# Kernel optimization log

Hardware: AMD Instinct MI355X
Metric: run time of the kernel (lower is better)

The kernel has to match this reference:

```python
import jax, jax.numpy as jnp
import numpy as np

DIM = 768
HEADS = 12
HEAD_DIM = DIM // HEADS
SCALE = HEAD_DIM ** -0.5


def setup_inputs() -> dict:
    key = jax.random.key(0)
    ks = jax.random.split(key, 7)
    B, N, C = 4, 1024, DIM
    s = 0.02
    return {
        "x": jax.random.normal(ks[0], (B, N, C), dtype=jnp.float32),
        "attn_mask": jax.random.normal(ks[1], (B, N, N), dtype=jnp.float32) * 0.1,
        "w_qkv": jax.random.normal(ks[2], (3 * C, C), dtype=jnp.float32) * s,
        "w_proj": jax.random.normal(ks[3], (C, C), dtype=jnp.float32) * s,
        "b_proj": jnp.zeros((C,), dtype=jnp.float32),
        "w_pre": jax.random.normal(ks[4], (HEADS, HEADS), dtype=jnp.float32) * 0.2,
        "w_post": jax.random.normal(ks[5], (HEADS, HEADS), dtype=jnp.float32) * 0.2,
    }


def reference(x, attn_mask, w_qkv, w_proj, b_proj, w_pre, w_post):
    B, N, C = x.shape
    H, D = HEADS, HEAD_DIM
    qkv = (x @ w_qkv.T).reshape(B, N, 3, H, D)
    q, k, v = jnp.moveaxis(qkv, 2, 0)          # each [B, N, H, D]
    q = q.transpose(0, 2, 1, 3)                # [B, H, N, D]
    k = k.transpose(0, 2, 1, 3)
    v = v.transpose(0, 2, 1, 3)
    attn = jnp.einsum("bhnd,bhmd->bhnm", q, k) * SCALE
    attn = attn + attn_mask[:, None, :, :]
    # talking-heads pre-softmax mixing: Linear over head axis (y = x @ W.T)
    attn = jnp.einsum("bhnm,gh->bgnm", attn, w_pre)
    attn = jax.nn.softmax(attn, axis=-1)
    # talking-heads post-softmax mixing
    attn = jnp.einsum("bhnm,gh->bgnm", attn, w_post)
    out = jnp.einsum("bhnm,bhmd->bhnd", attn, v)   # [B, H, N, D]
    out = out.transpose(0, 2, 1, 3).reshape(B, N, C)
    return out @ w_proj.T + b_proj
```

## Files before the change

### kernel.cpp

```cpp
#include <hip/hip_runtime.h>
#include <hip/hip_bf16.h>

typedef __attribute__((ext_vector_type(8))) short bf16x8;
typedef __attribute__((ext_vector_type(8))) short s16x8;
typedef __attribute__((ext_vector_type(4))) float f32x4;
typedef unsigned short u16;

__device__ __forceinline__ u16 f2bf(float f){
  __hip_bfloat16 h = __float2bfloat16(f);
  return *reinterpret_cast<u16*>(&h);
}
__device__ __forceinline__ float bf2f(u16 u){
  __hip_bfloat16 h;
  *reinterpret_cast<u16*>(&h) = u;
  return __bfloat162float(h);
}

__global__ __launch_bounds__(256) void cvt3_kernel(
    const float* __restrict__ s0, u16* __restrict__ d0, int n0,
    const float* __restrict__ s1, u16* __restrict__ d1, int n1,
    const float* __restrict__ s2, u16* __restrict__ d2, int n2)
{
  int i = blockIdx.x*256 + threadIdx.x;
  const float* s; u16* d; int idx; float sc = 1.f;
  if (i < n0){ s = s0; d = d0; idx = i; }
  else if (i < n0 + n1){
    idx = i - n0; s = s1; d = d1;
    if (idx < 768*192) sc = 0.125f;
  } else if (i < n0 + n1 + n2){
    idx = i - n0 - n1; s = s2; d = d2;
  } else return;
  float4 v = reinterpret_cast<const float4*>(s)[idx];
  ushort4 o;
  o.x = f2bf(v.x*sc); o.y = f2bf(v.y*sc); o.z = f2bf(v.z*sc); o.w = f2bf(v.w*sc);
  reinterpret_cast<ushort4*>(d)[idx] = o;
}

template<int BM, int BN, int MODE>
__global__ __launch_bounds__(256) void gemm_bt(
    const u16* __restrict__ A, const u16* __restrict__ B,
    void* __restrict__ C0, void* __restrict__ C1, void* __restrict__ C2,
    const float* __restrict__ bias,
    int M, int N, int K, int lda, int ldb, long sA, long sB, long sC)
{
  constexpr int BK = 32, LDT = 40;
  __shared__ u16 As[BM*LDT];
  __shared__ u16 Bs[BN*LDT];
  const int z = blockIdx.z;
  const u16* Ab = A + (long)z * sA;
  const u16* Bb = B + (long)z * sB;
  const int bm = blockIdx.x * BM, bn = blockIdx.y * BN;
  const int tid = threadIdx.x, lane = tid & 63, wv = tid >> 6;
  constexpr int WM = BM/2, WN = BN/2, FM = WM/16, FN = WN/16;
  const int wm = (wv >> 1) * WM, wn = (wv & 1) * WN;
  const int quad = lane >> 4, cl = lane & 15;
  f32x4 acc[FM][FN];
  #pragma unroll
  for (int i=0;i<FM;i++)
    #pragma unroll
    for (int j=0;j<FN;j++){ f32x4 zr = {0.f,0.f,0.f,0.f}; acc[i][j] = zr; }
  constexpr int AIT = (BM*BK)/(8*256);
  constexpr int BIT = (BN*BK)/(8*256);

  for (int kb = 0; kb < K; kb += BK){
    __syncthreads();
    #pragma unroll
    for (int sL=0; sL<AIT; sL++){
      int e = tid + sL*256, r = e >> 2, c8 = (e & 3) * 8;
      *reinterpret_cast<float4*>(&As[r*LDT + c8]) =
        *reinterpret_cast<const float4*>(Ab + (long)(bm + r)*lda + kb + c8);
    }
    #pragma unroll
    for (int sL=0; sL<BIT; sL++){
      int e = tid + sL*256, r = e >> 2, c8 = (e & 3) * 8;
      *reinterpret_cast<float4*>(&Bs[r*LDT + c8]) =
        *reinterpret_cast<const float4*>(Bb + (long)(bn + r)*ldb + kb + c8);
    }
    __syncthreads();
    bf16x8 af[FM], bfr[FN];
    #pragma unroll
    for (int i=0;i<FM;i++)
      af[i] = *reinterpret_cast<const bf16x8*>(&As[(wm + i*16 + cl)*LDT + quad*8]);
    #pragma unroll
    for (int j=0;j<FN;j++)
      bfr[j] = *reinterpret_cast<const bf16x8*>(&Bs[(wn + j*16 + cl)*LDT + quad*8]);
    #pragma unroll
    for (int i=0;i<FM;i++)
      #pragma unroll
      for (int j=0;j<FN;j++)
        acc[i][j] = __builtin_amdgcn_mfma_f32_16x16x32_bf16(af[i], bfr[j], acc[i][j], 0, 0, 0);
  }

  #pragma unroll
  for (int i=0;i<FM;i++)
  #pragma unroll
  for (int j=0;j<FN;j++)
  #pragma unroll
  for (int r=0;r<4;r++){
    int gm = bm + wm + i*16 + quad*4 + r;
    int gn = bn + wn + j*16 + cl;
    float v = acc[i][j][r];
    if (MODE == 0){
      int b_ = gm >> 10, n_ = gm & 1023;
      int t3 = (gn >= 1536) ? 2 : ((gn >= 768) ? 1 : 0);
      int rem = gn - t3*768;
      int h = rem >> 6, d = rem & 63;
      u16 hv = f2bf(v);
      if (t3 == 0)      ((u16*)C0)[((long)((b_*12 + h)*1024 + n_))*64 + d] = hv;
      else if (t3 == 1) ((u16*)C1)[((long)((b_*12 + h)*1024 + n_))*64 + d] = hv;
      else              ((u16*)C2)[((long)((b_*12 + h)*64 + d))*1024 + n_] = hv;
    } else if (MODE == 1){
      ((u16*)C0)[(long)z*sC + (long)gm*N + gn] = f2bf(v);
    } else if (MODE == 2){
      int b_ = z / 12, h = z - b_*12;
      ((u16*)C0)[((long)((b_*1024 + gm)*12 + h))*64 + gn] = f2bf(v);
    } else {
      ((float*)C0)[(long)gm*N + gn] = v + bias[gn];
    }
  }
}

__global__ __launch_bounds__(64, 2) void mix_kernel(
    u16* __restrict__ S, const float* __restrict__ mask,
    const float* __restrict__ w_pre, const float* __restrict__ w_post)
{
  const int bid = blockIdx.x;
  const int b = bid >> 10, n = bid & 1023;
  const int l = threadIdx.x;
  const long base0 = (((long)(b*12))*1024 + n) * 1024;
  const int off0 = l*8, off1 = 512 + l*8;

  float smix[12][16];

  #pragma unroll
  for (int h=0; h<12; h++){
    const u16* sr = S + base0 + (long)h*1024*1024;
    bf16x8 v0 = *reinterpret_cast<const bf16x8*>(sr + off0);
    bf16x8 v1 = *reinterpret_cast<const bf16x8*>(sr + off1);
    float sv[16];
    #pragma unroll
    for (int j=0;j<8;j++){ sv[j] = bf2f((u16)v0[j]); sv[8+j] = bf2f((u16)v1[j]); }
    if (h == 0){
      #pragma unroll
      for (int g=0;g<12;g++){
        float w = w_pre[g*12];
        #pragma unroll
        for (int mi=0;mi<16;mi++) smix[g][mi] = w * sv[mi];
      }
    } else {
      #pragma unroll
      for (int g=0;g<12;g++){
        float w = w_pre[g*12 + h];
        #pragma unroll
        for (int mi=0;mi<16;mi++) smix[g][mi] += w * sv[mi];
      }
    }
  }

  {
    const float* mr = mask + ((long)(b*1024 + n))*1024;
    float mk[16];
    float4 a0 = *reinterpret_cast<const float4*>(mr + off0);
    float4 a1 = *reinterpret_cast<const float4*>(mr + off0 + 4);
    float4 b0 = *reinterpret_cast<const float4*>(mr + off1);
    float4 b1 = *reinterpret_cast<const float4*>(mr + off1 + 4);
    mk[0]=a0.x; mk[1]=a0.y; mk[2]=a0.z; mk[3]=a0.w;
    mk[4]=a1.x; mk[5]=a1.y; mk[6]=a1.z; mk[7]=a1.w;
    mk[8]=b0.x; mk[9]=b0.y; mk[10]=b0.z; mk[11]=b0.w;
    mk[12]=b1.x; mk[13]=b1.y; mk[14]=b1.z; mk[15]=b1.w;
    #pragma unroll
    for (int g=0;g<12;g++){
      float rs = 0.f;
      #pragma unroll
      for (int h=0;h<12;h++) rs += w_pre[g*12 + h];
      #pragma unroll
      for (int mi=0;mi<16;mi++) smix[g][mi] += rs * mk[mi];
    }
  }

  float M[12];
  #pragma unroll
  for (int g=0;g<12;g++){
    float a = fmaxf(smix[g][0], smix[g][1]);
    float c = fmaxf(smix[g][2], smix[g][3]);
    float e = fmaxf(smix[g][4], smix[g][5]);
    float f = fmaxf(smix[g][6], smix[g][7]);
    float a2 = fmaxf(smix[g][8], smix[g][9]);
    float c2 = fmaxf(smix[g][10], smix[g][11]);
    float e2 = fmaxf(smix[g][12], smix[g][13]);
    float f2 = fmaxf(smix[g][14], smix[g][15]);
    M[g] = fmaxf(fmaxf(fmaxf(a,c), fmaxf(e,f)), fmaxf(fmaxf(a2,c2), fmaxf(e2,f2)));
  }
  #pragma unroll
  for (int off=32; off>0; off>>=1)
    #pragma unroll
    for (int g=0;g<12;g++) M[g] = fmaxf(M[g], __shfl_xor(M[g], off));

  float L[12];
  #pragma unroll
  for (int g=0;g<12;g++){
    float sum = 0.f;
    #pragma unroll
    for (int mi=0;mi<16;mi++){
      float e = __expf(smix[g][mi] - M[g]);
      smix[g][mi] = e; sum += e;
    }
    L[g] = sum;
  }
  #pragma unroll
  for (int off=32; off>0; off>>=1)
    #pragma unroll
    for (int g=0;g<12;g++) L[g] += __shfl_xor(L[g], off);
  #pragma unroll
  for (int g=0;g<12;g++){
    float inv = 1.0f / L[g];
    #pragma unroll
    for (int mi=0;mi<16;mi++) smix[g][mi] *= inv;
  }

  #pragma unroll
  for (int h=0; h<12; h++){
    float o[16];
    {
      float w = w_post[h*12];
      #pragma unroll
      for (int mi=0;mi<16;mi++) o[mi] = w * smix[0][mi];
    }
    #pragma unroll
    for (int g=1;g<12;g++){
      float w = w_post[h*12 + g];
      #pragma unroll
      for (int mi=0;mi<16;mi++) o[mi] += w * smix[g][mi];
    }
    s16x8 st0, st1;
    #pragma unroll
    for (int j=0;j<8;j++){
      st0[j] = (short)f2bf(o[j]);
      st1[j] = (short)f2bf(o[8+j]);
    }
    u16* orow = S + base0 + (long)h*1024*1024;
    *reinterpret_cast<s16x8*>(orow + off0) = st0;
    *reinterpret_cast<s16x8*>(orow + off1) = st1;
  }
}

extern "C" void kernel_launch(void* const* d_in, const int* in_sizes, int n_in,
                              void* d_out, int out_size, void* d_ws, size_t ws_size,
                              hipStream_t stream)
{
  const float* x      = (const float*)d_in[0];
  const float* mask   = (const float*)d_in[1];
  const float* w_qkv  = (const float*)d_in[2];
  const float* w_proj = (const float*)d_in[3];
  const float* b_proj = (const float*)d_in[4];
  const float* w_pre  = (const float*)d_in[5];
  const float* w_post = (const float*)d_in[6];
  float* out = (float*)d_out;

  u16* xb     = (u16*)d_ws;
  u16* wqkvb  = xb     + 4096l*768;
  u16* wprojb = wqkvb  + 2304l*768;
  u16* Qb     = wprojb + 768l*768;
  u16* Kb     = Qb     + 48l*1024*64;
  u16* Vtb    = Kb     + 48l*1024*64;
  u16* tmpb   = Vtb    + 48l*1024*64;
  u16* Sb     = tmpb   + 4096l*768;
  size_t need = ((size_t)(Sb - xb) + 48ul*1024*1024) * sizeof(u16);
  if (ws_size < need) return;

  const int n0 = 4096*768/4, n1 = 2304*768/4, n2 = 768*768/4;
  cvt3_kernel<<<(n0+n1+n2 + 255)/256, 256, 0, stream>>>(x, xb, n0, w_qkv, wqkvb, n1,
                                                        w_proj, wprojb, n2);

  dim3 gq(4096/128, 2304/128, 1);
  gemm_bt<128,128,0><<<gq, 256, 0, stream>>>(xb, wqkvb, Qb, Kb, Vtb, nullptr,
      4096, 2304, 768, 768, 768, 0, 0, 0);

  dim3 gs(1024/128, 1024/128, 48);
  gemm_bt<128,128,1><<<gs, 256, 0, stream>>>(Qb, Kb, Sb, nullptr, nullptr, nullptr,
      1024, 1024, 64, 64, 64, 1024l*64, 1024l*64, 1024l*1024);

  mix_kernel<<<4096, 64, 0, stream>>>(Sb, mask, w_pre, w_post);

  dim3 gp(1024/128, 1, 48);
  gemm_bt<128,64,2><<<gp, 256, 0, stream>>>(Sb, Vtb, tmpb, nullptr, nullptr, nullptr,
      1024, 64, 1024, 1024, 1024, 1024l*1024, 64l*1024, 0);

  dim3 go(4096/128, 768/128, 1);
  gemm_bt<128,128,3><<<go, 256, 0, stream>>>(tmpb, wprojb, out, nullptr, nullptr, b_proj,
      4096, 768, 768, 768, 768, 0, 0, 0);
}
```

Measured before the change: 293.4 us.

## Use direct global-to-LDS loads, widen mix kernel to two waves, shrink PV tile

The GEMM tile loads now use the global_load_lds builtin to copy straight into shared memory, with the LDS padding removed (LDT 32), so tiles no longer pass through registers. The mix kernel now runs 128 threads per row with 8 elements each, combines the two waves' max and sum through shared memory, and converts bf16 with shifts. The PV GEMM switches to 64x64 tiles for more blocks. Together these aim to cut register pressure, raise occupancy and reduce load latency, at the cost of possible LDS bank conflicts from the unpadded layout.

```diff
diff --git a/kernel.cpp b/kernel.cpp
--- a/kernel.cpp
+++ b/kernel.cpp
@@ -5,15 +5,19 @@
 typedef __attribute__((ext_vector_type(8))) short s16x8;
 typedef __attribute__((ext_vector_type(4))) float f32x4;
 typedef unsigned short u16;
+typedef unsigned int u32;
 
 __device__ __forceinline__ u16 f2bf(float f){
   __hip_bfloat16 h = __float2bfloat16(f);
   return *reinterpret_cast<u16*>(&h);
 }
-__device__ __forceinline__ float bf2f(u16 u){
-  __hip_bfloat16 h;
-  *reinterpret_cast<u16*>(&h) = u;
-  return __bfloat162float(h);
+__device__ __forceinline__ float bflo(u32 w){ return __uint_as_float(w << 16); }
+__device__ __forceinline__ float bfhi(u32 w){ return __uint_as_float(w & 0xffff0000u); }
+
+__device__ __forceinline__ void gload_lds16(const u16* g, u16* l){
+  __builtin_amdgcn_global_load_lds(
+      (__attribute__((address_space(1))) u32*)g,
+      (__attribute__((address_space(3))) u32*)l, 16, 0, 0);
 }
 
 __global__ __launch_bounds__(256) void cvt3_kernel(
@@ -43,9 +47,9 @@
     const float* __restrict__ bias,
     int M, int N, int K, int lda, int ldb, long sA, long sB, long sC)
 {
-  constexpr int BK = 32, LDT = 40;
-  __shared__ u16 As[BM*LDT];
-  __shared__ u16 Bs[BN*LDT];
+  constexpr int BK = 32, LDT = 32;
+  __shared__ __align__(16) u16 As[BM*LDT];
+  __shared__ __align__(16) u16 Bs[BN*LDT];
   const int z = blockIdx.z;
   const u16* Ab = A + (long)z * sA;
   const u16* Bb = B + (long)z * sB;
@@ -67,14 +71,12 @@
     #pragma unroll
     for (int sL=0; sL<AIT; sL++){
       int e = tid + sL*256, r = e >> 2, c8 = (e & 3) * 8;
-      *reinterpret_cast<float4*>(&As[r*LDT + c8]) =
-        *reinterpret_cast<const float4*>(Ab + (long)(bm + r)*lda + kb + c8);
+      gload_lds16(Ab + (long)(bm + r)*lda + kb + c8, &As[e*8]);
     }
     #pragma unroll
     for (int sL=0; sL<BIT; sL++){
       int e = tid + sL*256, r = e >> 2, c8 = (e & 3) * 8;
-      *reinterpret_cast<float4*>(&Bs[r*LDT + c8]) =
-        *reinterpret_cast<const float4*>(Bb + (long)(bn + r)*ldb + kb + c8);
+      gload_lds16(Bb + (long)(bn + r)*ldb + kb + c8, &Bs[e*8]);
     }
     __syncthreads();
     bf16x8 af[FM], bfr[FN];
@@ -120,88 +122,87 @@
   }
 }
 
-__global__ __launch_bounds__(64, 2) void mix_kernel(
+__global__ __launch_bounds__(128) __attribute__((amdgpu_waves_per_eu(3,3)))
+void mix_kernel(
     u16* __restrict__ S, const float* __restrict__ mask,
     const float* __restrict__ w_pre, const float* __restrict__ w_post)
 {
   const int bid = blockIdx.x;
   const int b = bid >> 10, n = bid & 1023;
-  const int l = threadIdx.x;
+  const int t = threadIdx.x;
+  const int wv = t >> 6, lane = t & 63;
+  const int moff = t * 8;
   const long base0 = (((long)(b*12))*1024 + n) * 1024;
-  const int off0 = l*8, off1 = 512 + l*8;
-
-  float smix[12][16];
+
+  float smix[12][8];
 
   #pragma unroll
   for (int h=0; h<12; h++){
-    const u16* sr = S + base0 + (long)h*1024*1024;
-    bf16x8 v0 = *reinterpret_cast<const bf16x8*>(sr + off0);
-    bf16x8 v1 = *reinterpret_cast<const bf16x8*>(sr + off1);
-    float sv[16];
-    #pragma unroll
-    for (int j=0;j<8;j++){ sv[j] = bf2f((u16)v0[j]); sv[8+j] = bf2f((u16)v1[j]); }
+    uint4 raw = *reinterpret_cast<const uint4*>(S + base0 + (long)h*1024*1024 + moff);
+    float sv[8];
+    sv[0]=bflo(raw.x); sv[1]=bfhi(raw.x);
+    sv[2]=bflo(raw.y); sv[3]=bfhi(raw.y);
+    sv[4]=bflo(raw.z); sv[5]=bfhi(raw.z);
+    sv[6]=bflo(raw.w); sv[7]=bfhi(raw.w);
     if (h == 0){
       #pragma unroll
       for (int g=0;g<12;g++){
         float w = w_pre[g*12];
         #pragma unroll
-        for (int mi=0;mi<16;mi++) smix[g][mi] = w * sv[mi];
+        for (int mi=0;mi<8;mi++) smix[g][mi] = w * sv[mi];
       }
     } else {
       #pragma unroll
       for (int g=0;g<12;g++){
         float w = w_pre[g*12 + h];
         #pragma unroll
-        for (int mi=0;mi<16;mi++) smix[g][mi] += w * sv[mi];
+        for (int mi=0;mi<8;mi++) smix[g][mi] += w * sv[mi];
       }
     }
   }
 
   {
-    const float* mr = mask + ((long)(b*1024 + n))*1024;
-    float mk[16];
-    float4 a0 = *reinterpret_cast<const float4*>(mr + off0);
-    float4 a1 = *reinterpret_cast<const float4*>(mr + off0 + 4);
-    float4 b0 = *reinterpret_cast<const float4*>(mr + off1);
-    float4 b1 = *reinterpret_cast<const float4*>(mr + off1 + 4);
-    mk[0]=a0.x; mk[1]=a0.y; mk[2]=a0.z; mk[3]=a0.w;
-    mk[4]=a1.x; mk[5]=a1.y; mk[6]=a1.z; mk[7]=a1.w;
-    mk[8]=b0.x; mk[9]=b0.y; mk[10]=b0.z; mk[11]=b0.w;
-    mk[12]=b1.x; mk[13]=b1.y; mk[14]=b1.z; mk[15]=b1.w;
+    const float* mr = mask + ((long)(b*1024 + n))*1024 + moff;
+    float4 a0 = *reinterpret_cast<const float4*>(mr);
+    float4 a1 = *reinterpret_cast<const float4*>(mr + 4);
+    float mk[8] = {a0.x,a0.y,a0.z,a0.w,a1.x,a1.y,a1.z,a1.w};
     #pragma unroll
     for (int g=0;g<12;g++){
       float rs = 0.f;
       #pragma unroll
       for (int h=0;h<12;h++) rs += w_pre[g*12 + h];
       #pragma unroll
-      for (int mi=0;mi<16;mi++) smix[g][mi] += rs * mk[mi];
-    }
-  }
-
+      for (int mi=0;mi<8;mi++) smix[g][mi] += rs * mk[mi];
+    }
+  }
+
+  __shared__ float redM[2][12];
+  __shared__ float redS[2][12];
   float M[12];
   #pragma unroll
   for (int g=0;g<12;g++){
-    float a = fmaxf(smix[g][0], smix[g][1]);
-    float c = fmaxf(smix[g][2], smix[g][3]);
-    float e = fmaxf(smix[g][4], smix[g][5]);
-    float f = fmaxf(smix[g][6], smix[g][7]);
-    float a2 = fmaxf(smix[g][8], smix[g][9]);
-    float c2 = fmaxf(smix[g][10], smix[g][11]);
-    float e2 = fmaxf(smix[g][12], smix[g][13]);
-    float f2 = fmaxf(smix[g][14], smix[g][15]);
-    M[g] = fmaxf(fmaxf(fmaxf(a,c), fmaxf(e,f)), fmaxf(fmaxf(a2,c2), fmaxf(e2,f2)));
+    float a = fmaxf(fmaxf(smix[g][0], smix[g][1]), fmaxf(smix[g][2], smix[g][3]));
+    float c = fmaxf(fmaxf(smix[g][4], smix[g][5]), fmaxf(smix[g][6], smix[g][7]));
+    M[g] = fmaxf(a, c);
   }
   #pragma unroll
   for (int off=32; off>0; off>>=1)
     #pragma unroll
     for (int g=0;g<12;g++) M[g] = fmaxf(M[g], __shfl_xor(M[g], off));
+  if (lane == 0){
+    #pragma unroll
+    for (int g=0;g<12;g++) redM[wv][g] = M[g];
+  }
+  __syncthreads();
+  #pragma unroll
+  for (int g=0;g<12;g++) M[g] = fmaxf(redM[0][g], redM[1][g]);
 
   float L[12];
   #pragma unroll
   for (int g=0;g<12;g++){
     float sum = 0.f;
     #pragma unroll
-    for (int mi=0;mi<16;mi++){
+    for (int mi=0;mi<8;mi++){
       float e = __expf(smix[g][mi] - M[g]);
       smix[g][mi] = e; sum += e;
     }
@@ -211,36 +212,36 @@
   for (int off=32; off>0; off>>=1)
     #pragma unroll
     for (int g=0;g<12;g++) L[g] += __shfl_xor(L[g], off);
+  if (lane == 0){
+    #pragma unroll
+    for (int g=0;g<12;g++) redS[wv][g] = L[g];
+  }
+  __syncthreads();
   #pragma unroll
   for (int g=0;g<12;g++){
-    float inv = 1.0f / L[g];
-    #pragma unroll
-    for (int mi=0;mi<16;mi++) smix[g][mi] *= inv;
+    float inv = 1.0f / (redS[0][g] + redS[1][g]);
+    #pragma unroll
+    for (int mi=0;mi<8;mi++) smix[g][mi] *= inv;
   }
 
   #pragma unroll
   for (int h=0; h<12; h++){
-    float o[16];
+    float o[8];
     {
       float w = w_post[h*12];
       #pragma unroll
-      for (int mi=0;mi<16;mi++) o[mi] = w * smix[0][mi];
+      for (int mi=0;mi<8;mi++) o[mi] = w * smix[0][mi];
     }
     #pragma unroll
     for (int g=1;g<12;g++){
       float w = w_post[h*12 + g];
       #pragma unroll
-      for (int mi=0;mi<16;mi++) o[mi] += w * smix[g][mi];
-    }
-    s16x8 st0, st1;
-    #pragma unroll
-    for (int j=0;j<8;j++){
-      st0[j] = (short)f2bf(o[j]);
-      st1[j] = (short)f2bf(o[8+j]);
-    }
-    u16* orow = S + base0 + (long)h*1024*1024;
-    *reinterpret_cast<s16x8*>(orow + off0) = st0;
-    *reinterpret_cast<s16x8*>(orow + off1) = st1;
+      for (int mi=0;mi<8;mi++) o[mi] += w * smix[g][mi];
+    }
+    s16x8 st;
+    #pragma unroll
+    for (int j=0;j<8;j++) st[j] = (short)f2bf(o[j]);
+    *reinterpret_cast<s16x8*>(S + base0 + (long)h*1024*1024 + moff) = st;
   }
 }
 
@@ -280,10 +281,10 @@
   gemm_bt<128,128,1><<<gs, 256, 0, stream>>>(Qb, Kb, Sb, nullptr, nullptr, nullptr,
       1024, 1024, 64, 64, 64, 1024l*64, 1024l*64, 1024l*1024);
 
-  mix_kernel<<<4096, 64, 0, stream>>>(Sb, mask, w_pre, w_post);
-
-  dim3 gp(1024/128, 1, 48);
-  gemm_bt<128,64,2><<<gp, 256, 0, stream>>>(Sb, Vtb, tmpb, nullptr, nullptr, nullptr,
+  mix_kernel<<<4096, 128, 0, stream>>>(Sb, mask, w_pre, w_post);
+
+  dim3 gp(1024/64, 1, 48);
+  gemm_bt<64,64,2><<<gp, 256, 0, stream>>>(Sb, Vtb, tmpb, nullptr, nullptr, nullptr,
       1024, 64, 1024, 1024, 1024, 1024l*1024, 64l*1024, 0);
 
   dim3 go(4096/128, 768/128, 1);
```

Result: faster. 264.7 us (-9.8%).
